# Kernel optimization log

Hardware: AMD Instinct MI355X
Metric: run time of the kernel (lower is better)

The kernel has to match this reference:

```python
import jax, jax.numpy as jnp
import numpy as np

T, B, D = 2048, 16, 1024


def _xavier(key, shape, gain):
    fan_in, fan_out = shape[1], shape[0]
    a = gain * np.sqrt(6.0 / (fan_in + fan_out))
    return jax.random.uniform(key, shape, jnp.float32, -a, a)


def setup_inputs() -> dict:
    key = jax.random.key(0)
    ks = jax.random.split(key, 4)
    return {
        "x": jax.random.normal(ks[0], (T, B, D), jnp.float32),
        "h0": jnp.zeros((B, D), jnp.float32),
        "A_log": jnp.full((D,), -2.0, jnp.float32),
        "r_delta": jnp.full((D,), 0.1, jnp.float32),
        "W_x": _xavier(ks[1], (D, D), 0.5),
        "W_delta": _xavier(ks[2], (D, D), 0.1),
        "W_gate": _xavier(ks[3], (D, D), 1.0),
        "b": jnp.zeros((D,), jnp.float32),
        "b_delta": jnp.full((D,), -2.0, jnp.float32),
        "b_gate": jnp.zeros((D,), jnp.float32),
    }


def reference(x, h0, A_log, r_delta, W_x, W_delta, W_gate, b, b_delta, b_gate):
    r_h = -jnp.exp(A_log)  # stable negative decay, [D]
    # Precompute the three input projections for all timesteps (one big GEMM each).
    xv = jnp.einsum("tbd,ed->tbe", x, W_x) + b          # [T,B,D]
    xd = jnp.einsum("tbd,ed->tbe", x, W_delta) + b_delta # [T,B,D]
    gate = jax.nn.silu(jnp.einsum("tbd,ed->tbe", x, W_gate) + b_gate)  # [T,B,D]

    def step(h_prev, inp):
        xv_t, xd_t = inp
        v = r_h * h_prev + xv_t
        delta = jax.nn.sigmoid(xd_t + r_delta * h_prev)
        h_new = (1.0 - delta) * h_prev + delta * jnp.tanh(v)
        return h_new, h_new

    _, hs = jax.lax.scan(step, h0, (xv, xd))  # hs: [T,B,D]
    output = hs * gate                        # [T,B,D]
    h = jnp.concatenate([h0[None], hs], axis=0)  # [T+1,B,D]
    return output, h
```

## Files before the change

kernel.cpp:

```cpp
#include <hip/hip_runtime.h>

#define T_DIM 2048
#define B_DIM 16
#define D_DIM 1024
#define M_DIM (T_DIM * B_DIM)
#define K2    2048
#define N3    3072

typedef unsigned short u16;
typedef __bf16 bf16x8 __attribute__((ext_vector_type(8)));
typedef float  f32x4  __attribute__((ext_vector_type(4)));

typedef __attribute__((address_space(3))) uint32_t       lds_u32_t;
typedef const __attribute__((address_space(1))) uint32_t glb_u32_t;

__device__ inline void gload16(const void* g, void* l) {
  __builtin_amdgcn_global_load_lds((glb_u32_t*)g, (lds_u32_t*)l, 16, 0, 0);
}

__device__ inline u16 f2bf_u(float f) {
  uint32_t u = __float_as_uint(f);
  uint32_t r = (u + 0x7FFFu + ((u >> 16) & 1u)) >> 16;
  return (u16)r;
}
__device__ inline float bfu2f(u16 u) {
  return __uint_as_float(((uint32_t)u) << 16);
}

__global__ void cvt_x_kernel(const float* __restrict__ x, u16* __restrict__ Xs) {
  int i = blockIdx.x * 256 + threadIdx.x;
  int m  = i >> 8;
  int c4 = (i & 255) << 2;
  float4 v = reinterpret_cast<const float4*>(x)[i];
  float f[4] = {v.x, v.y, v.z, v.w};
  u16 hi[4], lo[4];
#pragma unroll
  for (int j = 0; j < 4; ++j) {
    hi[j] = f2bf_u(f[j]);
    lo[j] = f2bf_u(f[j] - bfu2f(hi[j]));
  }
  u16* base = Xs + (size_t)m * K2 + c4;
  *reinterpret_cast<ushort4*>(base)        = make_ushort4(hi[0], hi[1], hi[2], hi[3]);
  *reinterpret_cast<ushort4*>(base + 1024) = make_ushort4(lo[0], lo[1], lo[2], lo[3]);
}

__global__ void cvt_w_kernel(const float* __restrict__ Wx, const float* __restrict__ Wd,
                             const float* __restrict__ Wg, u16* __restrict__ Ws) {
  int i = blockIdx.x * 256 + threadIdx.x;
  int n  = i >> 8;
  int c4 = (i & 255) << 2;
  const float* W = (n < 1024) ? Wx : (n < 2048 ? Wd : Wg);
  int row = n & 1023;
  float4 v = reinterpret_cast<const float4*>(W)[(size_t)row * 256 + (i & 255)];
  float f[4] = {v.x, v.y, v.z, v.w};
  u16 hi[4], lo[4];
#pragma unroll
  for (int j = 0; j < 4; ++j) {
    hi[j] = f2bf_u(f[j]);
    lo[j] = f2bf_u(f[j] - bfu2f(hi[j]));
  }
  u16* base = Ws + (size_t)n * K2 + c4;
  *reinterpret_cast<ushort4*>(base)        = make_ushort4(hi[0], hi[1], hi[2], hi[3]);
  *reinterpret_cast<ushort4*>(base + 1024) = make_ushort4(lo[0], lo[1], lo[2], lo[3]);
}

__global__ __launch_bounds__(256) void gemm_kernel(const u16* __restrict__ Xs,
                                                   const u16* __restrict__ Ws,
                                                   float* __restrict__ C) {
  __shared__ __align__(16) u16 As[128 * 64];
  __shared__ __align__(16) u16 Bs[128 * 64];

  int bid = blockIdx.x;
  int swz = (bid & 7) * 768 + (bid >> 3);
  int nt = swz >> 8;
  int mt = swz & 255;
  int tid  = threadIdx.x;
  int lane = tid & 63;
  int wid  = tid >> 6;
  int wr = wid >> 1, wc = wid & 1;
  int r16 = lane & 15, grp = lane >> 4;

  f32x4 acc[4][4];
#pragma unroll
  for (int m = 0; m < 4; ++m)
#pragma unroll
    for (int n = 0; n < 4; ++n)
#pragma unroll
      for (int e = 0; e < 4; ++e) acc[m][n][e] = 0.0f;

  const u16* Abase = Xs + (size_t)mt * 128 * K2;
  const u16* Bbase = Ws + (size_t)nt * 128 * K2;

#pragma unroll 1
  for (int p = 0; p < 3; ++p) {
    const u16* Ap = Abase + (p == 2 ? 1024 : 0);
    const u16* Bp = Bbase + (p == 1 ? 1024 : 0);
#pragma unroll 1
    for (int kt = 0; kt < 16; ++kt) {
      __syncthreads();
#pragma unroll
      for (int i = 0; i < 4; ++i) {
        int slot = i * 256 + tid;
        int row  = slot >> 3;
        int c    = (slot & 7) ^ (row & 7);
        gload16(Ap + (size_t)row * K2 + kt * 64 + c * 8,
                &As[(size_t)(i * 256 + wid * 64) * 8]);
      }
#pragma unroll
      for (int i = 0; i < 4; ++i) {
        int slot = i * 256 + tid;
        int row  = slot >> 3;
        int c    = (slot & 7) ^ (row & 7);
        gload16(Bp + (size_t)row * K2 + kt * 64 + c * 8,
                &Bs[(size_t)(i * 256 + wid * 64) * 8]);
      }
      __syncthreads();
#pragma unroll
      for (int ks = 0; ks < 2; ++ks) {
        bf16x8 af[4], bfr[4];
#pragma unroll
        for (int m = 0; m < 4; ++m) {
          int row = wr * 64 + m * 16 + r16;
          int ch  = (ks * 4 + grp) ^ (row & 7);
          af[m] = *reinterpret_cast<const bf16x8*>(&As[row * 64 + ch * 8]);
        }
#pragma unroll
        for (int n = 0; n < 4; ++n) {
          int row = wc * 64 + n * 16 + r16;
          int ch  = (ks * 4 + grp) ^ (row & 7);
          bfr[n] = *reinterpret_cast<const bf16x8*>(&Bs[row * 64 + ch * 8]);
        }
#pragma unroll
        for (int m = 0; m < 4; ++m)
#pragma unroll
          for (int n = 0; n < 4; ++n)
            acc[m][n] = __builtin_amdgcn_mfma_f32_16x16x32_bf16(af[m], bfr[n], acc[m][n], 0, 0, 0);
      }
    }
  }

  size_t baseRow = (size_t)mt * 128 + wr * 64 + grp * 4;
  int    baseCol = nt * 128 + wc * 64 + r16;
#pragma unroll
  for (int m = 0; m < 4; ++m)
#pragma unroll
    for (int reg = 0; reg < 4; ++reg) {
      float* crow = C + (baseRow + m * 16 + reg) * (size_t)N3 + baseCol;
#pragma unroll
      for (int n = 0; n < 4; ++n) crow[n * 16] = acc[m][n][reg];
    }
}

#define U_SC 16
__global__ __launch_bounds__(64) void scan_kernel(
    const float* __restrict__ C, const float* __restrict__ h0,
    const float* __restrict__ A_log, const float* __restrict__ r_delta,
    const float* __restrict__ bv, const float* __restrict__ bdl,
    const float* __restrict__ bgt, float* __restrict__ out) {
  int g = blockIdx.x * 64 + threadIdx.x;
  int d = g & 1023;
  float h  = h0[g];
  float rh = -__expf(A_log[d]);
  float rd = r_delta[d];
  float bb = bv[d], bd = bdl[d], bg = bgt[d];
  float* hout = out + (size_t)T_DIM * 16384;
  hout[g] = h;
  const float* Cb = C + (size_t)(g >> 10) * N3 + d;

  float pxv[U_SC], pxd[U_SC], pgp[U_SC];
#pragma unroll
  for (int u = 0; u < U_SC; ++u) {
    const float* cp = Cb + (size_t)u * 16 * N3;
    pxv[u] = cp[0]; pxd[u] = cp[1024]; pgp[u] = cp[2048];
  }

#pragma unroll 1
  for (int tg = 0; tg < T_DIM / U_SC; ++tg) {
    float cxv[U_SC], cxd[U_SC], cgp[U_SC];
#pragma unroll
    for (int u = 0; u < U_SC; ++u) { cxv[u] = pxv[u]; cxd[u] = pxd[u]; cgp[u] = pgp[u]; }
    if (tg + 1 < T_DIM / U_SC) {
      const float* nb = Cb + (size_t)(tg + 1) * U_SC * 16 * N3;
#pragma unroll
      for (int u = 0; u < U_SC; ++u) {
        const float* cp = nb + (size_t)u * 16 * N3;
        pxv[u] = cp[0]; pxd[u] = cp[1024]; pgp[u] = cp[2048];
      }
    }
#pragma unroll
    for (int u = 0; u < U_SC; ++u) {
      int t = tg * U_SC + u;
      float xv = cxv[u] + bb;
      float xd = cxd[u] + bd;
      float gp = cgp[u] + bg;
      float v     = fmaf(rh, h, xv);
      float delta = 1.0f / (1.0f + __expf(-(xd + rd * h)));
      float e2    = __expf(2.0f * v);
      float th    = 1.0f - 2.0f / (e2 + 1.0f);
      float hn    = fmaf(delta, th - h, h);
      float gate  = gp / (1.0f + __expf(-gp));
      __builtin_nontemporal_store(hn * gate, &out [(size_t)t       * 16384 + g]);
      __builtin_nontemporal_store(hn,        &hout[(size_t)(t + 1) * 16384 + g]);
      h = hn;
    }
  }
}

extern "C" void kernel_launch(void* const* d_in, const int* in_sizes, int n_in,
                              void* d_out, int out_size, void* d_ws, size_t ws_size,
                              hipStream_t stream) {
  const float* x       = (const float*)d_in[0];
  const float* h0      = (const float*)d_in[1];
  const float* A_log   = (const float*)d_in[2];
  const float* r_delta = (const float*)d_in[3];
  const float* W_x     = (const float*)d_in[4];
  const float* W_delta = (const float*)d_in[5];
  const float* W_gate  = (const float*)d_in[6];
  const float* b       = (const float*)d_in[7];
  const float* b_delta = (const float*)d_in[8];
  const float* b_gate  = (const float*)d_in[9];
  float* out = (float*)d_out;

  u16*   Xs = (u16*)d_ws;
  u16*   Ws = (u16*)((char*)d_ws + (size_t)M_DIM * K2 * 2);
  float* C  = (float*)((char*)d_ws + (size_t)M_DIM * K2 * 2 + (size_t)N3 * K2 * 2);

  hipLaunchKernelGGL(cvt_x_kernel, dim3(32768), dim3(256), 0, stream, x, Xs);
  hipLaunchKernelGGL(cvt_w_kernel, dim3(3072),  dim3(256), 0, stream, W_x, W_delta, W_gate, Ws);
  hipLaunchKernelGGL(gemm_kernel,  dim3(6144),  dim3(256), 0, stream, Xs, Ws, C);
  hipLaunchKernelGGL(scan_kernel,  dim3(256),   dim3(64),  0, stream,
                     C, h0, A_log, r_delta, b, b_delta, b_gate, out);
}
```

Measured before the change: 1.406 ms.

## Stage scan inputs through LDS via async global-to-LDS loads and fast reciprocals

The scan kernel stops prefetching the next 16 timesteps of projections into registers and instead double-buffers them in shared memory using direct global-to-LDS loads. The 48-register prefetch arrays go away, and the next group's loads overlap with the current group's compute. Divisions in sigmoid, tanh and silu become hardware reciprocal approximations, and the stores become ordinary rather than nontemporal. The trade-offs are an explicit vmcnt(0) wait per group that also waits on the 32 output stores, a small accuracy loss from the rcp approximation, and a changed cache policy on the outputs.

```diff
diff --git a/kernel.cpp b/kernel.cpp
--- a/kernel.cpp
+++ b/kernel.cpp
@@ -17,6 +17,9 @@
 __device__ inline void gload16(const void* g, void* l) {
   __builtin_amdgcn_global_load_lds((glb_u32_t*)g, (lds_u32_t*)l, 16, 0, 0);
 }
+__device__ inline void gload4(const void* g, void* l) {
+  __builtin_amdgcn_global_load_lds((glb_u32_t*)g, (lds_u32_t*)l, 4, 0, 0);
+}
 
 __device__ inline u16 f2bf_u(float f) {
   uint32_t u = __float_as_uint(f);
@@ -26,6 +29,8 @@
 __device__ inline float bfu2f(u16 u) {
   return __uint_as_float(((uint32_t)u) << 16);
 }
+
+__device__ inline float fast_rcp(float x) { return __builtin_amdgcn_rcpf(x); }
 
 __global__ void cvt_x_kernel(const float* __restrict__ x, u16* __restrict__ Xs) {
   int i = blockIdx.x * 256 + threadIdx.x;
@@ -151,58 +156,64 @@
     }
 }
 
-#define U_SC 16
+#define TG 16
 __global__ __launch_bounds__(64) void scan_kernel(
     const float* __restrict__ C, const float* __restrict__ h0,
     const float* __restrict__ A_log, const float* __restrict__ r_delta,
     const float* __restrict__ bv, const float* __restrict__ bdl,
     const float* __restrict__ bgt, float* __restrict__ out) {
-  int g = blockIdx.x * 64 + threadIdx.x;
+  __shared__ __align__(16) float sb[2][TG][3][64];
+  int tid = threadIdx.x;
+  int bid = blockIdx.x;
+  int g = bid * 64 + tid;
   int d = g & 1023;
+  int b = g >> 10;
   float h  = h0[g];
   float rh = -__expf(A_log[d]);
   float rd = r_delta[d];
   float bb = bv[d], bd = bdl[d], bg = bgt[d];
   float* hout = out + (size_t)T_DIM * 16384;
   hout[g] = h;
-  const float* Cb = C + (size_t)(g >> 10) * N3 + d;
-
-  float pxv[U_SC], pxd[U_SC], pgp[U_SC];
-#pragma unroll
-  for (int u = 0; u < U_SC; ++u) {
-    const float* cp = Cb + (size_t)u * 16 * N3;
-    pxv[u] = cp[0]; pxd[u] = cp[1024]; pgp[u] = cp[2048];
-  }
+  const float* Crow = C + (size_t)b * N3 + (d - tid) + tid;
+
+#pragma unroll
+  for (int u = 0; u < TG; ++u)
+#pragma unroll
+    for (int c = 0; c < 3; ++c)
+      gload4(Crow + ((size_t)u * 16) * N3 + c * 1024, &sb[0][u][c][0]);
+  asm volatile("s_waitcnt vmcnt(0)" ::: "memory");
+  __builtin_amdgcn_sched_barrier(0);
 
 #pragma unroll 1
-  for (int tg = 0; tg < T_DIM / U_SC; ++tg) {
-    float cxv[U_SC], cxd[U_SC], cgp[U_SC];
-#pragma unroll
-    for (int u = 0; u < U_SC; ++u) { cxv[u] = pxv[u]; cxd[u] = pxd[u]; cgp[u] = pgp[u]; }
-    if (tg + 1 < T_DIM / U_SC) {
-      const float* nb = Cb + (size_t)(tg + 1) * U_SC * 16 * N3;
-#pragma unroll
-      for (int u = 0; u < U_SC; ++u) {
-        const float* cp = nb + (size_t)u * 16 * N3;
-        pxv[u] = cp[0]; pxd[u] = cp[1024]; pgp[u] = cp[2048];
-      }
-    }
-#pragma unroll
-    for (int u = 0; u < U_SC; ++u) {
-      int t = tg * U_SC + u;
-      float xv = cxv[u] + bb;
-      float xd = cxd[u] + bd;
-      float gp = cgp[u] + bg;
+  for (int tg = 0; tg < T_DIM / TG; ++tg) {
+    int buf = tg & 1;
+    if (tg + 1 < T_DIM / TG) {
+      const float* nb = Crow + ((size_t)(tg + 1) * TG * 16) * N3;
+#pragma unroll
+      for (int u = 0; u < TG; ++u)
+#pragma unroll
+        for (int c = 0; c < 3; ++c)
+          gload4(nb + ((size_t)u * 16) * N3 + c * 1024, &sb[buf ^ 1][u][c][0]);
+    }
+#pragma unroll
+    for (int u = 0; u < TG; ++u) {
+      int t = tg * TG + u;
+      float xv = sb[buf][u][0][tid] + bb;
+      float xd = sb[buf][u][1][tid] + bd;
+      float gp = sb[buf][u][2][tid] + bg;
       float v     = fmaf(rh, h, xv);
-      float delta = 1.0f / (1.0f + __expf(-(xd + rd * h)));
+      float sarg  = fmaf(rd, h, xd);
+      float delta = fast_rcp(1.0f + __expf(-sarg));
       float e2    = __expf(2.0f * v);
-      float th    = 1.0f - 2.0f / (e2 + 1.0f);
+      float th    = fmaf(-2.0f, fast_rcp(e2 + 1.0f), 1.0f);
       float hn    = fmaf(delta, th - h, h);
-      float gate  = gp / (1.0f + __expf(-gp));
-      __builtin_nontemporal_store(hn * gate, &out [(size_t)t       * 16384 + g]);
-      __builtin_nontemporal_store(hn,        &hout[(size_t)(t + 1) * 16384 + g]);
+      float gate  = gp * fast_rcp(1.0f + __expf(-gp));
+      out [(size_t)t       * 16384 + g] = hn * gate;
+      hout[(size_t)(t + 1) * 16384 + g] = hn;
       h = hn;
     }
+    asm volatile("s_waitcnt vmcnt(0)" ::: "memory");
+    __builtin_amdgcn_sched_barrier(0);
   }
 }
 
```

New measurement: 1.265 ms. 1.11x faster.
